# Kernel optimization log

Hardware: AMD Instinct MI355X
Metric: run time of the kernel (lower is better)

## Reference

```python
import jax, jax.numpy as jnp
import numpy as np

B, C, T, H, W = 4, 256, 8, 32, 32
EPS = 1e-6


def setup_inputs() -> dict:
    key = jax.random.key(0)
    ks = jax.random.split(key, 8)
    s = 0.02  # init scale for 1x1 conv weights
    return {
        "x_motion": jax.random.normal(ks[0], (B, C, T, H, W), jnp.float32),
        "x_ref": jax.random.normal(ks[1], (B, C, 1, H, W), jnp.float32),
        "gamma": jnp.ones((C,), jnp.float32),
        "beta": jnp.zeros((C,), jnp.float32),
        "Wq": jax.random.normal(ks[2], (C, C), jnp.float32) * s,
        "bq": jnp.zeros((C,), jnp.float32),
        "Wk": jax.random.normal(ks[3], (C, C), jnp.float32) * s,
        "bk": jnp.zeros((C,), jnp.float32),
        "Wv": jax.random.normal(ks[4], (C, C), jnp.float32) * s,
        "bv": jnp.zeros((C,), jnp.float32),
        "Wo": jax.random.normal(ks[5], (C, C), jnp.float32) * s,
        "bo": jnp.zeros((C,), jnp.float32),
    }


def _group_norm(x, gamma, beta):
    # GroupNorm(num_groups=1): normalize over (C,T,H,W) per sample
    mu = jnp.mean(x, axis=(1, 2, 3, 4), keepdims=True)
    var = jnp.var(x, axis=(1, 2, 3, 4), keepdims=True)
    xn = (x - mu) * jax.lax.rsqrt(var + EPS)
    return xn * gamma[None, :, None, None, None] + beta[None, :, None, None, None]


def _conv1(x, Wmat, bias):
    # 1x1x1 Conv3d == per-position channel matmul
    return jnp.einsum('oc,bcthw->bothw', Wmat, x) + bias[None, :, None, None, None]


def reference(x_motion, x_ref, gamma, beta, Wq, bq, Wk, bk, Wv, bv, Wo, bo):
    h_mot = _group_norm(x_motion, gamma, beta)
    h_ref = _group_norm(x_ref, gamma, beta)
    q = _conv1(h_mot, Wq, bq)   # [b,c,t,h,w]
    k = _conv1(h_ref, Wk, bk)   # [b,c,1,h,w]
    v = _conv1(h_ref, Wv, bv)
    b, c, t, h, w = q.shape
    qf = q.transpose(0, 2, 3, 4, 1).reshape(b, t, h * w, c)   # [b,t,hw,c]
    kf = k[:, :, 0].transpose(0, 2, 3, 1).reshape(b, h * w, c)  # [b,hw,c]
    vf = v[:, :, 0].transpose(0, 2, 3, 1).reshape(b, h * w, c)
    # cross-attention: every frame attends to the single reference frame
    attn = jnp.einsum('btqc,bkc->btqk', qf, kf) * (c ** -0.5)
    attn = jax.nn.softmax(attn, axis=-1)
    out = jnp.einsum('btqk,bkc->btqc', attn, vf)
    out = out.reshape(b, t, h, w, c).transpose(0, 4, 1, 2, 3)  # [b,c,t,h,w]
    return x_motion + _conv1(out, Wo, bo)
```

## Files before the change

kernel.cpp:

```cpp
#include <hip/hip_runtime.h>
#include <math.h>
#include <stdint.h>

#define B_   4
#define C_   256
#define T_   8
#define HW_  1024
#define PM_  8192
#define PR_  1024
#define NM_  (C_ * PM_)
#define NR_  (C_ * PR_)
#define NBM  128
#define NBR  16
#define EPS_ 1e-6f
#define QSCALE 0.09016844f

typedef unsigned short u16;
typedef unsigned int u32;
typedef __attribute__((ext_vector_type(8))) short short8;
typedef __attribute__((ext_vector_type(4))) float f32x4;
typedef __attribute__((ext_vector_type(16))) float f32x16;

__device__ inline u16 f2bf(float f) {
    uint32_t u = __builtin_bit_cast(uint32_t, f);
    u += 0x7fffu + ((u >> 16) & 1u);
    return (u16)(u >> 16);
}
__device__ inline u32 pk2bf(float a, float b) {
    return (u32)f2bf(a) | ((u32)f2bf(b) << 16);
}

__device__ inline f32x4 mfma16(short8 a, short8 b, f32x4 c) {
    f32x4 d;
    asm("v_mfma_f32_16x16x32_bf16 %0, %1, %2, %3" : "=v"(d) : "v"(a), "v"(b), "0"(c));
    return d;
}
__device__ inline f32x16 mfma32(short8 a, short8 b, f32x16 c) {
    f32x16 d;
    asm("v_mfma_f32_32x32x16_bf16 %0, %1, %2, %3" : "=v"(d) : "v"(a), "v"(b), "0"(c));
    return d;
}
__device__ __forceinline__ short8 lds8(const char* p) {
    return __builtin_bit_cast(short8, *(const uint4*)p);
}
__device__ __forceinline__ void gl16(const void* g, void* l) {
    __builtin_amdgcn_global_load_lds(
        reinterpret_cast<const uint32_t __attribute__((address_space(1)))*>(
            reinterpret_cast<uintptr_t>(g)),
        reinterpret_cast<uint32_t __attribute__((address_space(3)))*>(
            reinterpret_cast<uintptr_t>(l)),
        16, 0, 0);
}

__device__ void gn_body(const float* __restrict__ x, int per_sample, int nblk,
                        float* __restrict__ part, int bid) {
    int b   = bid / nblk;
    int blk = bid % nblk;
    const float* xb = x + (size_t)b * per_sample;
    int chunk = per_sample / nblk;
    int base  = blk * chunk;
    float s = 0.f, s2 = 0.f;
    for (int i = threadIdx.x * 4; i < chunk; i += 256 * 4) {
        float4 v = *(const float4*)(xb + base + i);
        s  += v.x + v.y + v.z + v.w;
        s2 += v.x * v.x + v.y * v.y + v.z * v.z + v.w * v.w;
    }
    #pragma unroll
    for (int off = 32; off; off >>= 1) {
        s  += __shfl_down(s, off);
        s2 += __shfl_down(s2, off);
    }
    __shared__ float red[8];
    int wid = threadIdx.x >> 6, lane = threadIdx.x & 63;
    if (lane == 0) { red[wid * 2] = s; red[wid * 2 + 1] = s2; }
    __syncthreads();
    if (threadIdx.x == 0) {
        for (int w = 1; w < 4; ++w) { s += red[w * 2]; s2 += red[w * 2 + 1]; }
        part[(size_t)(b * nblk + blk) * 2]     = s;
        part[(size_t)(b * nblk + blk) * 2 + 1] = s2;
    }
}
__global__ __launch_bounds__(256) void gn_all(const float* __restrict__ xm,
                                              const float* __restrict__ xr,
                                              float* __restrict__ part_m,
                                              float* __restrict__ part_r) {
    if (blockIdx.x < 512) gn_body(xm, NM_, NBM, part_m, blockIdx.x);
    else                  gn_body(xr, NR_, NBR, part_r, blockIdx.x - 512);
}

__global__ __launch_bounds__(256) void fin_w2bf(const float* __restrict__ part_m,
                                                const float* __restrict__ part_r,
                                                const float* __restrict__ gamma,
                                                const float* __restrict__ beta,
                                                float* __restrict__ am, float* __restrict__ dm,
                                                float* __restrict__ ar, float* __restrict__ dr,
                                                const float* __restrict__ W0,
                                                const float* __restrict__ W1,
                                                const float* __restrict__ W2,
                                                const float* __restrict__ W3,
                                                u16* __restrict__ dst) {
    if (blockIdx.x == 128) {
        int c = threadIdx.x;
        float g = gamma[c], be = beta[c];
        for (int b = 0; b < B_; ++b) {
            float s = 0.f, s2 = 0.f;
            for (int i = 0; i < NBM; ++i) { s += part_m[(b * NBM + i) * 2]; s2 += part_m[(b * NBM + i) * 2 + 1]; }
            float mu   = s / (float)NM_;
            float var  = s2 / (float)NM_ - mu * mu;
            float rstd = rsqrtf(var + EPS_);
            am[b * C_ + c] = rstd * g;
            dm[b * C_ + c] = be - mu * rstd * g;

            s = 0.f; s2 = 0.f;
            for (int i = 0; i < NBR; ++i) { s += part_r[(b * NBR + i) * 2]; s2 += part_r[(b * NBR + i) * 2 + 1]; }
            mu   = s / (float)NR_;
            var  = s2 / (float)NR_ - mu * mu;
            rstd = rsqrtf(var + EPS_);
            ar[b * C_ + c] = rstd * g;
            dr[b * C_ + c] = be - mu * rstd * g;
        }
        return;
    }
    int idx = blockIdx.x * 256 + threadIdx.x;
    int m = idx >> 13, off = (idx & 8191) * 8;
    const float* s = (m == 0 ? W0 : m == 1 ? W1 : m == 2 ? W2 : W3) + off;
    float4 a = *(const float4*)s, b = *(const float4*)(s + 4);
    ushort4 lo; lo.x = f2bf(a.x); lo.y = f2bf(a.y); lo.z = f2bf(a.z); lo.w = f2bf(a.w);
    ushort4 hi; hi.x = f2bf(b.x); hi.y = f2bf(b.y); hi.z = f2bf(b.z); hi.w = f2bf(b.w);
    *(ushort4*)(dst + m * 65536 + off)     = lo;
    *(ushort4*)(dst + m * 65536 + off + 4) = hi;
}

__device__ void norm_body(const float* __restrict__ X,
                          const float* __restrict__ alpha,
                          const float* __restrict__ delta,
                          u16* __restrict__ Y, int P, int px, int b,
                          u16* S) {
    int p0 = px * 64;
    int tid = threadIdx.x;
    #pragma unroll
    for (int pass = 0; pass < 4; ++pass) {
        int qi = pass * 256 + tid;
        int cq = qi & 63, pq = qi >> 6;
        float4 v[4];
        #pragma unroll
        for (int j = 0; j < 4; ++j) {
            int c = cq * 4 + j;
            v[j] = *(const float4*)(X + ((size_t)b * C_ + c) * P + p0 + pq * 4);
            float a = alpha[b * C_ + c], d = delta[b * C_ + c];
            v[j].x = v[j].x * a + d; v[j].y = v[j].y * a + d;
            v[j].z = v[j].z * a + d; v[j].w = v[j].w * a + d;
        }
        #pragma unroll
        for (int jj = 0; jj < 4; ++jj) {
            ushort4 o;
            o.x = f2bf(((const float*)&v[0])[jj]);
            o.y = f2bf(((const float*)&v[1])[jj]);
            o.z = f2bf(((const float*)&v[2])[jj]);
            o.w = f2bf(((const float*)&v[3])[jj]);
            *(ushort4*)&S[(pq * 4 + jj) * 256 + cq * 4] = o;
        }
    }
    __syncthreads();
    const char* Sb = (const char*)S;
    #pragma unroll
    for (int pass = 0; pass < 8; ++pass) {
        int i = pass * 256 + tid;
        int p = i >> 5, s = i & 31;
        uint4 d = *(const uint4*)(Sb + p * 512 + s * 16);
        *(uint4*)((char*)(Y + ((size_t)b * P + p0 + p) * C_) + s * 16) = d;
    }
}
__global__ __launch_bounds__(256) void norm_all(const float* __restrict__ xm,
                                                const float* __restrict__ xr,
                                                const float* __restrict__ am,
                                                const float* __restrict__ dm,
                                                const float* __restrict__ ar,
                                                const float* __restrict__ dr,
                                                u16* __restrict__ xnm,
                                                u16* __restrict__ xnr) {
    __shared__ __align__(16) u16 S[64 * 256];
    int bid = blockIdx.x;
    if (bid < 512) norm_body(xm, am, dm, xnm, PM_, bid & 127, bid >> 7, S);
    else { int i = bid - 512; norm_body(xr, ar, dr, xnr, PR_, i & 15, i >> 4, S); }
}

template<int OUT>
__device__ void convA_body(char* lds,
                           const u16* __restrict__ Xb, const u16* __restrict__ Wb,
                           const float* __restrict__ bias, const float* __restrict__ resid,
                           void* __restrict__ Yv, int P, float oscale,
                           int px, int oy, int b) {
    int p0 = px * 64, o0 = oy * 64;
    int tid = threadIdx.x;
    int w = tid >> 6, l = tid & 63, lg = l >> 4, ln = l & 15;
    int wm = w >> 1, wn = w & 1;
    const char* Xg = (const char*)(Xb + ((size_t)b * P + p0) * C_);
    const char* Wg = (const char*)(Wb + (size_t)o0 * C_);
    #pragma unroll
    for (int i = 0; i < 8; ++i) {
        int ci = i * 4 + w;
        int d = ci * 1024 + l * 16;
        int srco = (d & ~511) | ((d & 511) ^ (((d >> 9) & 7) << 4));
        gl16(Xg + srco, lds + ci * 1024);
        gl16(Wg + srco, lds + 32768 + ci * 1024);
    }
    asm volatile("s_waitcnt vmcnt(0)" ::: "memory");
    __syncthreads();

    f32x4 acc[2][2];
    #pragma unroll
    for (int mm = 0; mm < 2; ++mm)
        #pragma unroll
        for (int nn = 0; nn < 2; ++nn) acc[mm][nn] = (f32x4)0.f;

    #pragma unroll
    for (int f = 0; f < 8; ++f) {
        short8 xf[2], wf[2];
        #pragma unroll
        for (int nn = 0; nn < 2; ++nn) {
            int p = wn * 32 + nn * 16 + ln;
            xf[nn] = lds8(lds + p * 512 + ((f * 64 + lg * 16) ^ ((p & 7) << 4)));
        }
        #pragma unroll
        for (int mm = 0; mm < 2; ++mm) {
            int o = wm * 32 + mm * 16 + ln;
            wf[mm] = lds8(lds + 32768 + o * 512 + ((f * 64 + lg * 16) ^ ((o & 7) << 4)));
        }
        #pragma unroll
        for (int mm = 0; mm < 2; ++mm)
            #pragma unroll
            for (int nn = 0; nn < 2; ++nn) {
                if (OUT == 1) acc[mm][nn] = mfma16(xf[nn], wf[mm], acc[mm][nn]);
                else          acc[mm][nn] = mfma16(wf[mm], xf[nn], acc[mm][nn]);
            }
    }
    __syncthreads();

    if constexpr (OUT == 0) {
        #pragma unroll
        for (int mm = 0; mm < 2; ++mm) {
            int obase = o0 + wm * 32 + mm * 16 + lg * 4;
            float b0 = bias[obase], b1 = bias[obase + 1], b2 = bias[obase + 2], b3 = bias[obase + 3];
            #pragma unroll
            for (int nn = 0; nn < 2; ++nn) {
                int pl = wn * 32 + nn * 16 + ln;
                int a = pl * 128 + ((wm * 64 + mm * 32 + lg * 8) ^ ((pl & 7) << 4));
                *(u32*)(lds + a)     = pk2bf((acc[mm][nn][0] + b0) * oscale, (acc[mm][nn][1] + b1) * oscale);
                *(u32*)(lds + a + 4) = pk2bf((acc[mm][nn][2] + b2) * oscale, (acc[mm][nn][3] + b3) * oscale);
            }
        }
        __syncthreads();
        u16* Y = (u16*)Yv;
        #pragma unroll
        for (int pass = 0; pass < 2; ++pass) {
            int i = pass * 256 + tid;
            int pl = i >> 3, s = i & 7;
            uint4 d = *(const uint4*)(lds + pl * 128 + ((s * 16) ^ ((pl & 7) << 4)));
            *(uint4*)(Y + (size_t)(b * P + p0 + pl) * C_ + o0 + s * 8) = d;
        }
    } else if constexpr (OUT == 1) {
        #pragma unroll
        for (int mm = 0; mm < 2; ++mm) {
            int ol = wm * 32 + mm * 16 + ln;
            float bo = bias[o0 + ol];
            #pragma unroll
            for (int nn = 0; nn < 2; ++nn) {
                int a = ol * 128 + ((wn * 64 + nn * 32 + lg * 8) ^ ((ol & 7) << 4));
                *(u32*)(lds + a)     = pk2bf(acc[mm][nn][0] + bo, acc[mm][nn][1] + bo);
                *(u32*)(lds + a + 4) = pk2bf(acc[mm][nn][2] + bo, acc[mm][nn][3] + bo);
            }
        }
        __syncthreads();
        u16* Y = (u16*)Yv;
        #pragma unroll
        for (int pass = 0; pass < 2; ++pass) {
            int i = pass * 256 + tid;
            int ol = i >> 3, s = i & 7;
            uint4 d = *(const uint4*)(lds + ol * 128 + ((s * 16) ^ ((ol & 7) << 4)));
            *(uint4*)(Y + (size_t)(b * C_ + o0 + ol) * P + p0 + s * 8) = d;
        }
    } else {
        #pragma unroll
        for (int mm = 0; mm < 2; ++mm) {
            int obase = wm * 32 + mm * 16 + lg * 4;
            #pragma unroll
            for (int r = 0; r < 4; ++r) {
                int ol = obase + r;
                float bo = bias[o0 + ol];
                #pragma unroll
                for (int nn = 0; nn < 2; ++nn) {
                    int a = ol * 256 + ((wn * 128 + nn * 64 + ln * 4) ^ ((ol & 7) << 4));
                    *(float*)(lds + a) = acc[mm][nn][r] + bo;
                }
            }
        }
        __syncthreads();
        float* Y = (float*)Yv;
        #pragma unroll
        for (int pass = 0; pass < 4; ++pass) {
            int i = pass * 256 + tid;
            int ol = i >> 4, s = i & 15;
            f32x4 dv = *(const f32x4*)(lds + ol * 256 + ((s * 16) ^ ((ol & 7) << 4)));
            size_t go = (size_t)(b * C_ + o0 + ol) * P + p0 + s * 4;
            float4 rv = *(const float4*)(resid + go);
            float4 o4;
            o4.x = dv[0] + rv.x; o4.y = dv[1] + rv.y; o4.z = dv[2] + rv.z; o4.w = dv[3] + rv.w;
            *(float4*)(Y + go) = o4;
        }
    }
}

__global__ __launch_bounds__(256) void convQKV(const u16* __restrict__ xnm,
                                               const u16* __restrict__ xnr,
                                               const u16* __restrict__ wall,
                                               const float* __restrict__ bq,
                                               const float* __restrict__ bk,
                                               const float* __restrict__ bv,
                                               u16* __restrict__ qT,
                                               u16* __restrict__ kT,
                                               u16* __restrict__ vh) {
    __shared__ __align__(16) char lds[65536];
    int bid = blockIdx.x;
    if (bid < 2048) {
        convA_body<0>(lds, xnm, wall, bq, nullptr, qT, PM_, QSCALE,
                      bid & 127, (bid >> 7) & 3, bid >> 9);
    } else if (bid < 2304) {
        int i = bid - 2048;
        convA_body<0>(lds, xnr, wall + 65536, bk, nullptr, kT, PR_, 1.f,
                      i & 15, (i >> 4) & 3, i >> 6);
    } else {
        int i = bid - 2304;
        convA_body<1>(lds, xnr, wall + 131072, bv, nullptr, vh, PR_, 1.f,
                      i & 15, (i >> 4) & 3, i >> 6);
    }
}

__global__ __launch_bounds__(256) void convO(const u16* __restrict__ aoh,
                                             const u16* __restrict__ wall,
                                             const float* __restrict__ bo,
                                             const float* __restrict__ resid,
                                             float* __restrict__ out) {
    __shared__ __align__(16) char lds[65536];
    convA_body<2>(lds, aoh, wall + 196608, bo, resid, out, PM_, 1.f,
                  blockIdx.x, blockIdx.y, blockIdx.z);
}

__global__ __launch_bounds__(256, 1) void attn4(const u16* __restrict__ qT,
                                                const u16* __restrict__ kT,
                                                const u16* __restrict__ vh,
                                                u16* __restrict__ ao) {
    __shared__ __align__(16) char lds[147456];
    int b = blockIdx.z, t = blockIdx.y, q0 = blockIdx.x * 128;
    int tid = threadIdx.x, w = tid >> 6, l = tid & 63;
    int m31 = l & 31, hi = l >> 5;

    const char* Kb = (const char*)(kT + (size_t)b * PR_ * C_);
    const char* Vb = (const char*)(vh + (size_t)b * C_ * PR_);

    auto stage = [&](int buf, int kt) {
        char* Kl = lds + buf * 32768;
        char* Vl = lds + 65536 + buf * 32768;
        #pragma unroll
        for (int i = 0; i < 8; ++i) {
            int ci = i * 4 + w;
            int d = ci * 1024 + l * 16;
            int srco = (d & ~511) | ((d & 511) ^ (((d >> 9) & 7) << 4));
            gl16(Kb + (size_t)kt * 32768 + srco, Kl + ci * 1024);
        }
        #pragma unroll
        for (int i = 0; i < 8; ++i) {
            int ci = i * 4 + w;
            int d = ci * 1024 + l * 16;
            int c = d >> 7, s = (d >> 4) & 7;
            int srco = c * 2048 + kt * 128 + ((s * 16) ^ ((c & 7) << 4));
            gl16(Vb + srco, Vl + ci * 1024);
        }
    };

    stage(0, 0);

    const char* Qrow = (const char*)(qT + ((size_t)b * PM_ + t * HW_ + q0 + w * 32 + m31) * C_);
    short8 qf[16];
    #pragma unroll
    for (int ch = 0; ch < 16; ++ch)
        qf[ch] = __builtin_bit_cast(short8, *(const uint4*)(Qrow + ch * 32 + hi * 16));

    f32x16 acc[8];
    #pragma unroll
    for (int cb = 0; cb < 8; ++cb) acc[cb] = (f32x16)0.f;
    float m_r = -1e30f, l_r = 0.f;

    asm volatile("s_waitcnt vmcnt(0)" ::: "memory");
    __syncthreads();

    char* Pw = lds + 131072 + w * 4096;
    int swzp = (m31 & 7) << 4;

    for (int kt = 0; kt < 16; ++kt) {
        int buf = kt & 1;
        if (kt < 15) stage(buf ^ 1, kt + 1);
        const char* Kl = lds + buf * 32768;
        const char* Vl = lds + 65536 + buf * 32768;

        f32x16 s0 = (f32x16)0.f, s1 = (f32x16)0.f;
        #pragma unroll
        for (int ch = 0; ch < 16; ++ch) {
            int off = (ch * 32 + hi * 16) ^ swzp;
            short8 k0f = lds8(Kl + m31 * 512 + off);
            short8 k1f = lds8(Kl + (32 + m31) * 512 + off);
            s0 = mfma32(k0f, qf[ch], s0);
            s1 = mfma32(k1f, qf[ch], s1);
        }

        float tm = -1e30f;
        #pragma unroll
        for (int e = 0; e < 16; ++e) tm = fmaxf(tm, fmaxf(s0[e], s1[e]));
        if (__any(tm > m_r + 8.f)) {
            float tmax = fmaxf(tm, __shfl_xor(tm, 32));
            float mn = fmaxf(m_r, tmax);
            float sc = __builtin_amdgcn_exp2f(m_r - mn);
            l_r *= sc;
            #pragma unroll
            for (int cb = 0; cb < 8; ++cb)
                #pragma unroll
                for (int e = 0; e < 16; ++e) acc[cb][e] *= sc;
            m_r = mn;
        }
        float p0[16], p1[16], rs = 0.f;
        #pragma unroll
        for (int e = 0; e < 16; ++e) { p0[e] = __builtin_amdgcn_exp2f(s0[e] - m_r); rs += p0[e]; }
        #pragma unroll
        for (int e = 0; e < 16; ++e) { p1[e] = __builtin_amdgcn_exp2f(s1[e] - m_r); rs += p1[e]; }
        l_r += rs;

        #pragma unroll
        for (int a = 0; a < 8; ++a) {
            const float* parr = (a < 4) ? p0 : p1;
            int eb = (a & 3) * 4;
            uint2 d;
            d.x = pk2bf(parr[eb + 0], parr[eb + 1]);
            d.y = pk2bf(parr[eb + 2], parr[eb + 3]);
            *(uint2*)(Pw + m31 * 128 + ((a * 16 + hi * 8) ^ swzp)) = d;
        }

        short8 bP[4];
        #pragma unroll
        for (int kc = 0; kc < 4; ++kc)
            bP[kc] = lds8(Pw + m31 * 128 + ((kc * 32 + hi * 16) ^ swzp));

        #pragma unroll
        for (int cb = 0; cb < 8; ++cb) {
            int c = cb * 32 + m31;
            int rowb = c * 128, swzc = (c & 7) << 4;
            #pragma unroll
            for (int kc = 0; kc < 4; ++kc) {
                short8 vf = lds8(Vl + rowb + ((kc * 32 + hi * 16) ^ swzc));
                acc[cb] = mfma32(vf, bP[kc], acc[cb]);
            }
        }

        asm volatile("s_waitcnt vmcnt(0)" ::: "memory");
        __syncthreads();
    }

    l_r += __shfl_xor(l_r, 32);
    float invl = 1.f / l_r;
    char* Os = lds;
    int q = w * 32 + m31;
    int swzq = (q & 7) << 4;
    #pragma unroll
    for (int cb = 0; cb < 8; ++cb)
        #pragma unroll
        for (int m = 0; m < 4; ++m) {
            uint2 d;
            d.x = pk2bf(acc[cb][4 * m + 0] * invl, acc[cb][4 * m + 1] * invl);
            d.y = pk2bf(acc[cb][4 * m + 2] * invl, acc[cb][4 * m + 3] * invl);
            *(uint2*)(Os + q * 512 + ((cb * 64 + m * 16 + hi * 8) ^ swzq)) = d;
        }
    __syncthreads();
    u16* aob = ao + ((size_t)b * PM_ + t * HW_ + q0) * C_;
    #pragma unroll
    for (int pass = 0; pass < 16; ++pass) {
        int i = pass * 256 + tid;
        int qr = i >> 5, s = i & 31;
        uint4 d = *(const uint4*)(Os + qr * 512 + ((s * 16) ^ ((qr & 7) << 4)));
        *(uint4*)((char*)(aob + (size_t)qr * C_) + s * 16) = d;
    }
}

extern "C" void kernel_launch(void* const* d_in, const int* in_sizes, int n_in,
                              void* d_out, int out_size, void* d_ws, size_t ws_size,
                              hipStream_t stream) {
    const float* x_motion = (const float*)d_in[0];
    const float* x_ref    = (const float*)d_in[1];
    const float* gamma    = (const float*)d_in[2];
    const float* beta     = (const float*)d_in[3];
    const float* Wq = (const float*)d_in[4];
    const float* bq = (const float*)d_in[5];
    const float* Wk = (const float*)d_in[6];
    const float* bk = (const float*)d_in[7];
    const float* Wv = (const float*)d_in[8];
    const float* bv = (const float*)d_in[9];
    const float* Wo = (const float*)d_in[10];
    const float* bo = (const float*)d_in[11];
    float* out = (float*)d_out;
    char* base = (char*)d_ws;

    float* part_m = (float*)(base);
    float* part_r = (float*)(base + 4096);
    float* am = (float*)(base + 8192);
    float* dm = (float*)(base + 12288);
    float* ar = (float*)(base + 16384);
    float* dr = (float*)(base + 20480);
    u16* wall = (u16*)(base + 32768);
    u16* xnm = (u16*)(base + 1048576);
    u16* aoh = xnm;
    u16* xnr = (u16*)(base + 1048576 + 16777216);
    u16* qT  = (u16*)(base + 1048576 + 16777216 + 2097152);
    u16* kTp = (u16*)(base + 1048576 + 2 * 16777216 + 2097152);
    u16* vh  = (u16*)(base + 1048576 + 2 * 16777216 + 2 * 2097152);

    gn_all<<<dim3(576), 256, 0, stream>>>(x_motion, x_ref, part_m, part_r);
    fin_w2bf<<<dim3(129), 256, 0, stream>>>(part_m, part_r, gamma, beta,
                                            am, dm, ar, dr, Wq, Wk, Wv, Wo, wall);
    norm_all<<<dim3(576), 256, 0, stream>>>(x_motion, x_ref, am, dm, ar, dr, xnm, xnr);
    convQKV<<<dim3(2560), 256, 0, stream>>>(xnm, xnr, wall, bq, bk, bv, qT, kTp, vh);
    attn4<<<dim3(8, T_, B_), 256, 0, stream>>>(qT, kTp, vh, aoh);
    convO<<<dim3(PM_ / 64, 4, B_), 256, 0, stream>>>(aoh, wall, bo, x_motion, out);
}
```

Baseline: 127.6 us.

## Compute all output channels per conv block to reuse input tile

```diff
diff --git a/kernel.cpp b/kernel.cpp
--- a/kernel.cpp
+++ b/kernel.cpp
@@ -186,127 +186,145 @@
 }
 
 template<int OUT>
-__device__ void convA_body(char* lds,
+__device__ void convB_body(char* lds,
                            const u16* __restrict__ Xb, const u16* __restrict__ Wb,
                            const float* __restrict__ bias, const float* __restrict__ resid,
                            void* __restrict__ Yv, int P, float oscale,
-                           int px, int oy, int b) {
-    int p0 = px * 64, o0 = oy * 64;
+                           int px, int b) {
+    int p0 = px * 64;
     int tid = threadIdx.x;
     int w = tid >> 6, l = tid & 63, lg = l >> 4, ln = l & 15;
     int wm = w >> 1, wn = w & 1;
     const char* Xg = (const char*)(Xb + ((size_t)b * P + p0) * C_);
-    const char* Wg = (const char*)(Wb + (size_t)o0 * C_);
     #pragma unroll
     for (int i = 0; i < 8; ++i) {
         int ci = i * 4 + w;
         int d = ci * 1024 + l * 16;
         int srco = (d & ~511) | ((d & 511) ^ (((d >> 9) & 7) << 4));
         gl16(Xg + srco, lds + ci * 1024);
-        gl16(Wg + srco, lds + 32768 + ci * 1024);
-    }
-    asm volatile("s_waitcnt vmcnt(0)" ::: "memory");
-    __syncthreads();
-
-    f32x4 acc[2][2];
-    #pragma unroll
-    for (int mm = 0; mm < 2; ++mm)
-        #pragma unroll
-        for (int nn = 0; nn < 2; ++nn) acc[mm][nn] = (f32x4)0.f;
-
-    #pragma unroll
-    for (int f = 0; f < 8; ++f) {
-        short8 xf[2], wf[2];
-        #pragma unroll
-        for (int nn = 0; nn < 2; ++nn) {
-            int p = wn * 32 + nn * 16 + ln;
-            xf[nn] = lds8(lds + p * 512 + ((f * 64 + lg * 16) ^ ((p & 7) << 4)));
-        }
-        #pragma unroll
-        for (int mm = 0; mm < 2; ++mm) {
-            int o = wm * 32 + mm * 16 + ln;
-            wf[mm] = lds8(lds + 32768 + o * 512 + ((f * 64 + lg * 16) ^ ((o & 7) << 4)));
-        }
+    }
+
+    f32x4 acc[4][2][2];
+    #pragma unroll
+    for (int oy = 0; oy < 4; ++oy)
         #pragma unroll
         for (int mm = 0; mm < 2; ++mm)
             #pragma unroll
+            for (int nn = 0; nn < 2; ++nn) acc[oy][mm][nn] = (f32x4)0.f;
+
+    #pragma unroll
+    for (int oy = 0; oy < 4; ++oy) {
+        const char* Wg = (const char*)(Wb + (size_t)(oy * 64) * C_);
+        #pragma unroll
+        for (int i = 0; i < 8; ++i) {
+            int ci = i * 4 + w;
+            int d = ci * 1024 + l * 16;
+            int srco = (d & ~511) | ((d & 511) ^ (((d >> 9) & 7) << 4));
+            gl16(Wg + srco, lds + 32768 + ci * 1024);
+        }
+        asm volatile("s_waitcnt vmcnt(0)" ::: "memory");
+        __syncthreads();
+        #pragma unroll
+        for (int f = 0; f < 8; ++f) {
+            short8 xf[2], wf[2];
+            #pragma unroll
             for (int nn = 0; nn < 2; ++nn) {
-                if (OUT == 1) acc[mm][nn] = mfma16(xf[nn], wf[mm], acc[mm][nn]);
-                else          acc[mm][nn] = mfma16(wf[mm], xf[nn], acc[mm][nn]);
-            }
-    }
-    __syncthreads();
-
-    if constexpr (OUT == 0) {
-        #pragma unroll
-        for (int mm = 0; mm < 2; ++mm) {
-            int obase = o0 + wm * 32 + mm * 16 + lg * 4;
-            float b0 = bias[obase], b1 = bias[obase + 1], b2 = bias[obase + 2], b3 = bias[obase + 3];
-            #pragma unroll
-            for (int nn = 0; nn < 2; ++nn) {
-                int pl = wn * 32 + nn * 16 + ln;
-                int a = pl * 128 + ((wm * 64 + mm * 32 + lg * 8) ^ ((pl & 7) << 4));
-                *(u32*)(lds + a)     = pk2bf((acc[mm][nn][0] + b0) * oscale, (acc[mm][nn][1] + b1) * oscale);
-                *(u32*)(lds + a + 4) = pk2bf((acc[mm][nn][2] + b2) * oscale, (acc[mm][nn][3] + b3) * oscale);
-            }
+                int p = wn * 32 + nn * 16 + ln;
+                xf[nn] = lds8(lds + p * 512 + ((f * 64 + lg * 16) ^ ((p & 7) << 4)));
+            }
+            #pragma unroll
+            for (int mm = 0; mm < 2; ++mm) {
+                int o = wm * 32 + mm * 16 + ln;
+                wf[mm] = lds8(lds + 32768 + o * 512 + ((f * 64 + lg * 16) ^ ((o & 7) << 4)));
+            }
+            #pragma unroll
+            for (int mm = 0; mm < 2; ++mm)
+                #pragma unroll
+                for (int nn = 0; nn < 2; ++nn) {
+                    if (OUT == 1) acc[oy][mm][nn] = mfma16(xf[nn], wf[mm], acc[oy][mm][nn]);
+                    else          acc[oy][mm][nn] = mfma16(wf[mm], xf[nn], acc[oy][mm][nn]);
+                }
         }
         __syncthreads();
-        u16* Y = (u16*)Yv;
-        #pragma unroll
-        for (int pass = 0; pass < 2; ++pass) {
-            int i = pass * 256 + tid;
-            int pl = i >> 3, s = i & 7;
-            uint4 d = *(const uint4*)(lds + pl * 128 + ((s * 16) ^ ((pl & 7) << 4)));
-            *(uint4*)(Y + (size_t)(b * P + p0 + pl) * C_ + o0 + s * 8) = d;
-        }
-    } else if constexpr (OUT == 1) {
-        #pragma unroll
-        for (int mm = 0; mm < 2; ++mm) {
-            int ol = wm * 32 + mm * 16 + ln;
-            float bo = bias[o0 + ol];
-            #pragma unroll
-            for (int nn = 0; nn < 2; ++nn) {
-                int a = ol * 128 + ((wn * 64 + nn * 32 + lg * 8) ^ ((ol & 7) << 4));
-                *(u32*)(lds + a)     = pk2bf(acc[mm][nn][0] + bo, acc[mm][nn][1] + bo);
-                *(u32*)(lds + a + 4) = pk2bf(acc[mm][nn][2] + bo, acc[mm][nn][3] + bo);
-            }
-        }
-        __syncthreads();
-        u16* Y = (u16*)Yv;
-        #pragma unroll
-        for (int pass = 0; pass < 2; ++pass) {
-            int i = pass * 256 + tid;
-            int ol = i >> 3, s = i & 7;
-            uint4 d = *(const uint4*)(lds + ol * 128 + ((s * 16) ^ ((ol & 7) << 4)));
-            *(uint4*)(Y + (size_t)(b * C_ + o0 + ol) * P + p0 + s * 8) = d;
-        }
-    } else {
-        #pragma unroll
-        for (int mm = 0; mm < 2; ++mm) {
-            int obase = wm * 32 + mm * 16 + lg * 4;
-            #pragma unroll
-            for (int r = 0; r < 4; ++r) {
-                int ol = obase + r;
+    }
+
+    #pragma unroll
+    for (int oy = 0; oy < 4; ++oy) {
+        int o0 = oy * 64;
+        if constexpr (OUT == 0) {
+            #pragma unroll
+            for (int mm = 0; mm < 2; ++mm) {
+                int obase = o0 + wm * 32 + mm * 16 + lg * 4;
+                float b0 = bias[obase], b1 = bias[obase + 1], b2 = bias[obase + 2], b3 = bias[obase + 3];
+                #pragma unroll
+                for (int nn = 0; nn < 2; ++nn) {
+                    int pl = wn * 32 + nn * 16 + ln;
+                    int a = pl * 128 + ((wm * 64 + mm * 32 + lg * 8) ^ ((pl & 7) << 4));
+                    *(u32*)(lds + a)     = pk2bf((acc[oy][mm][nn][0] + b0) * oscale, (acc[oy][mm][nn][1] + b1) * oscale);
+                    *(u32*)(lds + a + 4) = pk2bf((acc[oy][mm][nn][2] + b2) * oscale, (acc[oy][mm][nn][3] + b3) * oscale);
+                }
+            }
+            __syncthreads();
+            u16* Y = (u16*)Yv;
+            #pragma unroll
+            for (int pass = 0; pass < 2; ++pass) {
+                int i = pass * 256 + tid;
+                int pl = i >> 3, s = i & 7;
+                uint4 d = *(const uint4*)(lds + pl * 128 + ((s * 16) ^ ((pl & 7) << 4)));
+                *(uint4*)(Y + (size_t)(b * P + p0 + pl) * C_ + o0 + s * 8) = d;
+            }
+            __syncthreads();
+        } else if constexpr (OUT == 1) {
+            #pragma unroll
+            for (int mm = 0; mm < 2; ++mm) {
+                int ol = wm * 32 + mm * 16 + ln;
                 float bo = bias[o0 + ol];
                 #pragma unroll
                 for (int nn = 0; nn < 2; ++nn) {
-                    int a = ol * 256 + ((wn * 128 + nn * 64 + ln * 4) ^ ((ol & 7) << 4));
-                    *(float*)(lds + a) = acc[mm][nn][r] + bo;
+                    int a = ol * 128 + ((wn * 64 + nn * 32 + lg * 8) ^ ((ol & 7) << 4));
+                    *(u32*)(lds + a)     = pk2bf(acc[oy][mm][nn][0] + bo, acc[oy][mm][nn][1] + bo);
+                    *(u32*)(lds + a + 4) = pk2bf(acc[oy][mm][nn][2] + bo, acc[oy][mm][nn][3] + bo);
                 }
             }
-        }
-        __syncthreads();
-        float* Y = (float*)Yv;
-        #pragma unroll
-        for (int pass = 0; pass < 4; ++pass) {
-            int i = pass * 256 + tid;
-            int ol = i >> 4, s = i & 15;
-            f32x4 dv = *(const f32x4*)(lds + ol * 256 + ((s * 16) ^ ((ol & 7) << 4)));
-            size_t go = (size_t)(b * C_ + o0 + ol) * P + p0 + s * 4;
-            float4 rv = *(const float4*)(resid + go);
-            float4 o4;
-            o4.x = dv[0] + rv.x; o4.y = dv[1] + rv.y; o4.z = dv[2] + rv.z; o4.w = dv[3] + rv.w;
-            *(float4*)(Y + go) = o4;
+            __syncthreads();
+            u16* Y = (u16*)Yv;
+            #pragma unroll
+            for (int pass = 0; pass < 2; ++pass) {
+                int i = pass * 256 + tid;
+                int ol = i >> 3, s = i & 7;
+                uint4 d = *(const uint4*)(lds + ol * 128 + ((s * 16) ^ ((ol & 7) << 4)));
+                *(uint4*)(Y + (size_t)(b * C_ + o0 + ol) * P + p0 + s * 8) = d;
+            }
+            __syncthreads();
+        } else {
+            #pragma unroll
+            for (int mm = 0; mm < 2; ++mm) {
+                int obase = wm * 32 + mm * 16 + lg * 4;
+                #pragma unroll
+                for (int r = 0; r < 4; ++r) {
+                    int ol = obase + r;
+                    float bo = bias[o0 + ol];
+                    #pragma unroll
+                    for (int nn = 0; nn < 2; ++nn) {
+                        int a = ol * 256 + ((wn * 128 + nn * 64 + ln * 4) ^ ((ol & 7) << 4));
+                        *(float*)(lds + a) = acc[oy][mm][nn][r] + bo;
+                    }
+                }
+            }
+            __syncthreads();
+            float* Y = (float*)Yv;
+            #pragma unroll
+            for (int pass = 0; pass < 4; ++pass) {
+                int i = pass * 256 + tid;
+                int ol = i >> 4, s = i & 15;
+                f32x4 dv = *(const f32x4*)(lds + ol * 256 + ((s * 16) ^ ((ol & 7) << 4)));
+                size_t go = (size_t)(b * C_ + o0 + ol) * P + p0 + s * 4;
+                float4 rv = *(const float4*)(resid + go);
+                float4 o4;
+                o4.x = dv[0] + rv.x; o4.y = dv[1] + rv.y; o4.z = dv[2] + rv.z; o4.w = dv[3] + rv.w;
+                *(float4*)(Y + go) = o4;
+            }
+            __syncthreads();
         }
     }
 }
@@ -322,17 +340,14 @@
                                                u16* __restrict__ vh) {
     __shared__ __align__(16) char lds[65536];
     int bid = blockIdx.x;
-    if (bid < 2048) {
-        convA_body<0>(lds, xnm, wall, bq, nullptr, qT, PM_, QSCALE,
-                      bid & 127, (bid >> 7) & 3, bid >> 9);
-    } else if (bid < 2304) {
-        int i = bid - 2048;
-        convA_body<0>(lds, xnr, wall + 65536, bk, nullptr, kT, PR_, 1.f,
-                      i & 15, (i >> 4) & 3, i >> 6);
+    if (bid < 512) {
+        convB_body<0>(lds, xnm, wall, bq, nullptr, qT, PM_, QSCALE, bid & 127, bid >> 7);
+    } else if (bid < 576) {
+        int i = bid - 512;
+        convB_body<0>(lds, xnr, wall + 65536, bk, nullptr, kT, PR_, 1.f, i & 15, i >> 4);
     } else {
-        int i = bid - 2304;
-        convA_body<1>(lds, xnr, wall + 131072, bv, nullptr, vh, PR_, 1.f,
-                      i & 15, (i >> 4) & 3, i >> 6);
+        int i = bid - 576;
+        convB_body<1>(lds, xnr, wall + 131072, bv, nullptr, vh, PR_, 1.f, i & 15, i >> 4);
     }
 }
 
@@ -342,8 +357,8 @@
                                              const float* __restrict__ resid,
                                              float* __restrict__ out) {
     __shared__ __align__(16) char lds[65536];
-    convA_body<2>(lds, aoh, wall + 196608, bo, resid, out, PM_, 1.f,
-                  blockIdx.x, blockIdx.y, blockIdx.z);
+    convB_body<2>(lds, aoh, wall + 196608, bo, resid, out, PM_, 1.f,
+                  blockIdx.x, blockIdx.z);
 }
 
 __global__ __launch_bounds__(256, 1) void attn4(const u16* __restrict__ qT,
@@ -443,6 +458,8 @@
             d.y = pk2bf(parr[eb + 2], parr[eb + 3]);
             *(uint2*)(Pw + m31 * 128 + ((a * 16 + hi * 8) ^ swzp)) = d;
         }
+
+        asm volatile("" ::: "memory");
 
         short8 bP[4];
         #pragma unroll
@@ -525,7 +542,7 @@
     fin_w2bf<<<dim3(129), 256, 0, stream>>>(part_m, part_r, gamma, beta,
                                             am, dm, ar, dr, Wq, Wk, Wv, Wo, wall);
     norm_all<<<dim3(576), 256, 0, stream>>>(x_motion, x_ref, am, dm, ar, dr, xnm, xnr);
-    convQKV<<<dim3(2560), 256, 0, stream>>>(xnm, xnr, wall, bq, bk, bv, qT, kTp, vh);
+    convQKV<<<dim3(640), 256, 0, stream>>>(xnm, xnr, wall, bq, bk, bv, qT, kTp, vh);
     attn4<<<dim3(8, T_, B_), 256, 0, stream>>>(qT, kTp, vh, aoh);
-    convO<<<dim3(PM_ / 64, 4, B_), 256, 0, stream>>>(aoh, wall, bo, x_motion, out);
-}
+    convO<<<dim3(128, 1, B_), 256, 0, stream>>>(aoh, wall, bo, x_motion, out);
+}
```

After: 137.6 us. +7.8%, slower.
